# Performance work log

Hardware: AMD Instinct MI355X
Metric: run time of the kernel (lower is better)

## Reference

```python
import jax, jax.numpy as jnp
import numpy as np

MARGIN = 0.2
NEG_INF = -1e30
POS_INF = 1e30


def setup_inputs() -> dict:
    key = jax.random.key(0)
    k1, k2 = jax.random.split(key)
    B, D = 8192, 128
    im = jax.random.normal(k1, (B, D), dtype=jnp.float32)
    ids = jax.random.randint(k2, (B,), 0, 512, dtype=jnp.int64)
    return {"im": im, "ids": ids}


def reference(im, ids):
    # scores[i, j] = <im_i, im_j>, with the diagonal zeroed (as in the original,
    # which sets scores[j][j] = 0 before mining). Note the positive set includes
    # the anchor itself, so min over positives includes the zeroed diagonal.
    B = im.shape[0]
    scores = im @ im.T                      # [B, B]
    scores = scores * (1.0 - jnp.eye(B, dtype=scores.dtype))
    pos_mask = ids[:, None] == ids[None, :]  # same id (includes self)
    neg_mask = ~pos_mask
    max_neg = jnp.max(jnp.where(neg_mask, scores, NEG_INF), axis=1)  # hardest negative per anchor
    min_pos = jnp.min(jnp.where(pos_mask, scores, POS_INF), axis=1)  # hardest positive per anchor
    cost = jnp.sum(jnp.maximum(MARGIN + max_neg - min_pos, 0.0))
    return cost
```

## Files before the change

kernel.cpp:

```cpp
#include <hip/hip_runtime.h>
#include <hip/hip_bf16.h>

#define MARGIN  0.2f
#define NEG_INF -1e30f
#define POS_INF 1e30f

#define B_SZ 8192
#define D_SZ 128
#define CS   16
#define BLK_COLS 512
#define PHASE_COLS 64
#define NPH (BLK_COLS / PHASE_COLS)
#define NBUF 3

typedef __bf16 bf16x8 __attribute__((ext_vector_type(8)));
typedef float  f32x4  __attribute__((ext_vector_type(4)));
typedef float  f32x16 __attribute__((ext_vector_type(16)));

__global__ __launch_bounds__(256) void k_convert(const float* __restrict__ in,
                                                 __bf16* __restrict__ out) {
    int i = (blockIdx.x * 256 + threadIdx.x) * 8;
    float4 v0 = *reinterpret_cast<const float4*>(in + i);
    float4 v1 = *reinterpret_cast<const float4*>(in + i + 4);
    bf16x8 o;
    o[0] = (__bf16)v0.x; o[1] = (__bf16)v0.y; o[2] = (__bf16)v0.z; o[3] = (__bf16)v0.w;
    o[4] = (__bf16)v1.x; o[5] = (__bf16)v1.y; o[6] = (__bf16)v1.z; o[7] = (__bf16)v1.w;
    *reinterpret_cast<bf16x8*>(out + i) = o;
}

__global__ __launch_bounds__(256, 3) void k_mine(const __bf16* __restrict__ imb,
                                                 const int* __restrict__ ids,
                                                 float* __restrict__ wsmax,
                                                 float* __restrict__ wsmin) {
    __shared__ __bf16 bpanel[NBUF][PHASE_COLS * D_SZ];

    const int bid = blockIdx.x;
    const int wg  = (bid & 7) * 128 + (bid >> 3);
    const int rb  = wg & 63;
    const int cs  = wg >> 6;

    const int tid  = threadIdx.x;
    const int w    = tid >> 6;
    const int lane = tid & 63;
    const int half = lane >> 5;
    const int l5   = lane & 31;

    const int rowbase = rb * 128 + w * 32;
    const int col0    = cs * BLK_COLS;

    const int s_tile = w >> 1;
    const int s_kf0  = (w & 1) * 4;

    bf16x8 afrag[8];
    {
        const __bf16* p = imb + (size_t)(rowbase + l5) * D_SZ + half * 8;
        #pragma unroll
        for (int kf = 0; kf < 8; ++kf)
            afrag[kf] = *reinterpret_cast<const bf16x8*>(p + kf * 16);
    }
    int rid[16];
    #pragma unroll
    for (int r = 0; r < 16; ++r)
        rid[r] = ids[rowbase + (r & 3) + 8 * (r >> 2) + 4 * half];

    #pragma unroll
    for (int pp = 0; pp < 2; ++pp) {
        const __bf16* src = imb + (size_t)(col0 + pp * PHASE_COLS + s_tile * 32 + l5) * D_SZ
                            + s_kf0 * 16 + half * 8;
        #pragma unroll
        for (int j = 0; j < 4; ++j)
            __builtin_amdgcn_global_load_lds(
                (const __attribute__((address_space(1))) unsigned int*)(src + j * 16),
                (__attribute__((address_space(3))) unsigned int*)(&bpanel[pp][(s_tile * 8 + s_kf0 + j) * 512]),
                16, 0, 0);
    }
    asm volatile("s_waitcnt vmcnt(4)" ::: "memory");
    __builtin_amdgcn_s_barrier();

    float mxn[16], mnp[16];
    #pragma unroll
    for (int r = 0; r < 16; ++r) { mxn[r] = NEG_INF; mnp[r] = POS_INF; }

    #pragma unroll 1
    for (int p = 0; p < NPH; ++p) {
        if (p + 2 < NPH) {
            const int bs = (p + 2) % NBUF;
            const __bf16* src = imb + (size_t)(col0 + (p + 2) * PHASE_COLS + s_tile * 32 + l5) * D_SZ
                                + s_kf0 * 16 + half * 8;
            #pragma unroll
            for (int j = 0; j < 4; ++j)
                __builtin_amdgcn_global_load_lds(
                    (const __attribute__((address_space(1))) unsigned int*)(src + j * 16),
                    (__attribute__((address_space(3))) unsigned int*)(&bpanel[bs][(s_tile * 8 + s_kf0 + j) * 512]),
                    16, 0, 0);
        }
        const int buf = p % NBUF;
        #pragma unroll
        for (int t = 0; t < 2; ++t) {
            const __bf16* bbase = &bpanel[buf][t * 4096] + (size_t)lane * 8;
            f32x16 acc = {};
            #pragma unroll
            for (int kf = 0; kf < 8; ++kf) {
                bf16x8 bfr = *reinterpret_cast<const bf16x8*>(bbase + kf * 512);
                acc = __builtin_amdgcn_mfma_f32_32x32x16_bf16(afrag[kf], bfr, acc, 0, 0, 0);
            }
            const int cid = ids[col0 + p * PHASE_COLS + t * 32 + l5];
            #pragma unroll
            for (int r = 0; r < 16; ++r) {
                float sv   = acc[r];
                bool  same = (rid[r] == cid);
                mxn[r] = fmaxf(mxn[r], same ? NEG_INF : sv);
                mnp[r] = fminf(mnp[r], same ? sv : POS_INF);
            }
        }
        if (p + 2 < NPH) {
            asm volatile("s_waitcnt vmcnt(4)" ::: "memory");
        } else {
            asm volatile("s_waitcnt vmcnt(0)" ::: "memory");
        }
        __builtin_amdgcn_s_barrier();
    }

    #pragma unroll
    for (int r = 0; r < 16; ++r) {
        float mx = mxn[r];
        float mn = mnp[r];
        #pragma unroll
        for (int m = 1; m < 32; m <<= 1) {
            mx = fmaxf(mx, __shfl_xor(mx, m, 64));
            mn = fminf(mn, __shfl_xor(mn, m, 64));
        }
        if (l5 == 0) {
            int row = rowbase + (r & 3) + 8 * (r >> 2) + 4 * half;
            wsmax[(size_t)row * CS + cs] = mx;
            wsmin[(size_t)row * CS + cs] = mn;
        }
    }
}

__global__ __launch_bounds__(256) void k_final(const float* __restrict__ wsmax,
                                               const float* __restrict__ wsmin,
                                               float* __restrict__ out) {
    int r = blockIdx.x * 256 + threadIdx.x;
    float mx = NEG_INF;
    float mn = 0.0f;
    #pragma unroll
    for (int c = 0; c < CS; c += 4) {
        f32x4 vx = *reinterpret_cast<const f32x4*>(wsmax + (size_t)r * CS + c);
        f32x4 vn = *reinterpret_cast<const f32x4*>(wsmin + (size_t)r * CS + c);
        mx = fmaxf(mx, fmaxf(fmaxf(vx[0], vx[1]), fmaxf(vx[2], vx[3])));
        mn = fminf(mn, fminf(fminf(vn[0], vn[1]), fminf(vn[2], vn[3])));
    }
    float cost = fmaxf(MARGIN + mx - mn, 0.0f);
    #pragma unroll
    for (int m = 1; m < 64; m <<= 1)
        cost += __shfl_xor(cost, m, 64);
    __shared__ float part[4];
    if ((threadIdx.x & 63) == 0) part[threadIdx.x >> 6] = cost;
    __syncthreads();
    if (threadIdx.x == 0)
        atomicAdd(out, part[0] + part[1] + part[2] + part[3]);
}

extern "C" void kernel_launch(void* const* d_in, const int* in_sizes, int n_in,
                              void* d_out, int out_size, void* d_ws, size_t ws_size,
                              hipStream_t stream) {
    const float* im  = (const float*)d_in[0];
    const int*   ids = (const int*)d_in[1];
    float*       out = (float*)d_out;

    __bf16* imb   = (__bf16*)d_ws;
    float*  wsmax = (float*)((char*)d_ws + (size_t)B_SZ * D_SZ * 2);
    float*  wsmin = wsmax + (size_t)B_SZ * CS;

    hipMemsetAsync(d_out, 0, sizeof(float), stream);

    k_convert<<<(B_SZ * D_SZ) / (256 * 8), 256, 0, stream>>>(im, imb);
    k_mine<<<64 * CS, 256, 0, stream>>>(imb, ids, wsmax, wsmin);
    k_final<<<B_SZ / 256, 256, 0, stream>>>(wsmax, wsmin, out);
}
```

Baseline: 98.65 us.

## Reshape warp tiling to 64x32 per wave so B fragments are reused across two A tiles

Each wave now computes two 32-row subtiles against one 32-column tile, reusing each LDS B fragment for two MFMAs instead of loading it once per MFMA. Column ids are staged in shared memory once per block instead of being read from global memory per phase. Register pressure doubles for A fragments and accumulators, so launch bounds drop to 2 blocks per CU. The partial-result workspace widens to 32 partials per row to hold the per-wave column split.

```diff
diff --git a/kernel.cpp b/kernel.cpp
--- a/kernel.cpp
+++ b/kernel.cpp
@@ -8,6 +8,7 @@
 #define B_SZ 8192
 #define D_SZ 128
 #define CS   16
+#define PCS  32
 #define BLK_COLS 512
 #define PHASE_COLS 64
 #define NPH (BLK_COLS / PHASE_COLS)
@@ -28,11 +29,12 @@
     *reinterpret_cast<bf16x8*>(out + i) = o;
 }
 
-__global__ __launch_bounds__(256, 3) void k_mine(const __bf16* __restrict__ imb,
+__global__ __launch_bounds__(256, 2) void k_mine(const __bf16* __restrict__ imb,
                                                  const int* __restrict__ ids,
                                                  float* __restrict__ wsmax,
                                                  float* __restrict__ wsmin) {
     __shared__ __bf16 bpanel[NBUF][PHASE_COLS * D_SZ];
+    __shared__ int    ids_s[BLK_COLS];
 
     const int bid = blockIdx.x;
     const int wg  = (bid & 7) * 128 + (bid >> 3);
@@ -45,23 +47,32 @@
     const int half = lane >> 5;
     const int l5   = lane & 31;
 
-    const int rowbase = rb * 128 + w * 32;
+    const int h = w >> 1;
+    const int c = w & 1;
+
+    const int rowbase = rb * 128 + h * 64;
     const int col0    = cs * BLK_COLS;
 
     const int s_tile = w >> 1;
     const int s_kf0  = (w & 1) * 4;
 
-    bf16x8 afrag[8];
-    {
-        const __bf16* p = imb + (size_t)(rowbase + l5) * D_SZ + half * 8;
+    *reinterpret_cast<int2*>(&ids_s[tid * 2]) =
+        *reinterpret_cast<const int2*>(ids + col0 + tid * 2);
+
+    bf16x8 afrag[2][8];
+    #pragma unroll
+    for (int st = 0; st < 2; ++st) {
+        const __bf16* p = imb + (size_t)(rowbase + st * 32 + l5) * D_SZ + half * 8;
         #pragma unroll
         for (int kf = 0; kf < 8; ++kf)
-            afrag[kf] = *reinterpret_cast<const bf16x8*>(p + kf * 16);
+            afrag[st][kf] = *reinterpret_cast<const bf16x8*>(p + kf * 16);
     }
-    int rid[16];
+    int rid[2][16];
     #pragma unroll
-    for (int r = 0; r < 16; ++r)
-        rid[r] = ids[rowbase + (r & 3) + 8 * (r >> 2) + 4 * half];
+    for (int st = 0; st < 2; ++st)
+        #pragma unroll
+        for (int r = 0; r < 16; ++r)
+            rid[st][r] = ids[rowbase + st * 32 + (r & 3) + 8 * (r >> 2) + 4 * half];
 
     #pragma unroll
     for (int pp = 0; pp < 2; ++pp) {
@@ -74,12 +85,14 @@
                 (__attribute__((address_space(3))) unsigned int*)(&bpanel[pp][(s_tile * 8 + s_kf0 + j) * 512]),
                 16, 0, 0);
     }
-    asm volatile("s_waitcnt vmcnt(4)" ::: "memory");
+    asm volatile("s_waitcnt vmcnt(4) lgkmcnt(0)" ::: "memory");
     __builtin_amdgcn_s_barrier();
 
-    float mxn[16], mnp[16];
+    float mxn[2][16], mnp[2][16];
     #pragma unroll
-    for (int r = 0; r < 16; ++r) { mxn[r] = NEG_INF; mnp[r] = POS_INF; }
+    for (int st = 0; st < 2; ++st)
+        #pragma unroll
+        for (int r = 0; r < 16; ++r) { mxn[st][r] = NEG_INF; mnp[st][r] = POS_INF; }
 
     #pragma unroll 1
     for (int p = 0; p < NPH; ++p) {
@@ -95,23 +108,25 @@
                     16, 0, 0);
         }
         const int buf = p % NBUF;
+        const int cid = ids_s[p * PHASE_COLS + c * 32 + l5];
+
+        const __bf16* bbase = &bpanel[buf][c * 8 * 512] + (size_t)lane * 8;
+        f32x16 acc0 = {}, acc1 = {};
         #pragma unroll
-        for (int t = 0; t < 2; ++t) {
-            const __bf16* bbase = &bpanel[buf][t * 4096] + (size_t)lane * 8;
-            f32x16 acc = {};
-            #pragma unroll
-            for (int kf = 0; kf < 8; ++kf) {
-                bf16x8 bfr = *reinterpret_cast<const bf16x8*>(bbase + kf * 512);
-                acc = __builtin_amdgcn_mfma_f32_32x32x16_bf16(afrag[kf], bfr, acc, 0, 0, 0);
-            }
-            const int cid = ids[col0 + p * PHASE_COLS + t * 32 + l5];
-            #pragma unroll
-            for (int r = 0; r < 16; ++r) {
-                float sv   = acc[r];
-                bool  same = (rid[r] == cid);
-                mxn[r] = fmaxf(mxn[r], same ? NEG_INF : sv);
-                mnp[r] = fminf(mnp[r], same ? sv : POS_INF);
-            }
+        for (int kf = 0; kf < 8; ++kf) {
+            bf16x8 bfr = *reinterpret_cast<const bf16x8*>(bbase + kf * 512);
+            acc0 = __builtin_amdgcn_mfma_f32_32x32x16_bf16(afrag[0][kf], bfr, acc0, 0, 0, 0);
+            acc1 = __builtin_amdgcn_mfma_f32_32x32x16_bf16(afrag[1][kf], bfr, acc1, 0, 0, 0);
+        }
+        #pragma unroll
+        for (int r = 0; r < 16; ++r) {
+            float s0 = acc0[r], s1 = acc1[r];
+            bool  m0 = (rid[0][r] == cid);
+            bool  m1 = (rid[1][r] == cid);
+            mxn[0][r] = fmaxf(mxn[0][r], m0 ? NEG_INF : s0);
+            mnp[0][r] = fminf(mnp[0][r], m0 ? s0 : POS_INF);
+            mxn[1][r] = fmaxf(mxn[1][r], m1 ? NEG_INF : s1);
+            mnp[1][r] = fminf(mnp[1][r], m1 ? s1 : POS_INF);
         }
         if (p + 2 < NPH) {
             asm volatile("s_waitcnt vmcnt(4)" ::: "memory");
@@ -122,20 +137,22 @@
     }
 
     #pragma unroll
-    for (int r = 0; r < 16; ++r) {
-        float mx = mxn[r];
-        float mn = mnp[r];
+    for (int st = 0; st < 2; ++st)
         #pragma unroll
-        for (int m = 1; m < 32; m <<= 1) {
-            mx = fmaxf(mx, __shfl_xor(mx, m, 64));
-            mn = fminf(mn, __shfl_xor(mn, m, 64));
+        for (int r = 0; r < 16; ++r) {
+            float mx = mxn[st][r];
+            float mn = mnp[st][r];
+            #pragma unroll
+            for (int m = 1; m < 32; m <<= 1) {
+                mx = fmaxf(mx, __shfl_xor(mx, m, 64));
+                mn = fminf(mn, __shfl_xor(mn, m, 64));
+            }
+            if (l5 == 0) {
+                int row = rowbase + st * 32 + (r & 3) + 8 * (r >> 2) + 4 * half;
+                wsmax[(size_t)row * PCS + cs * 2 + c] = mx;
+                wsmin[(size_t)row * PCS + cs * 2 + c] = mn;
+            }
         }
-        if (l5 == 0) {
-            int row = rowbase + (r & 3) + 8 * (r >> 2) + 4 * half;
-            wsmax[(size_t)row * CS + cs] = mx;
-            wsmin[(size_t)row * CS + cs] = mn;
-        }
-    }
 }
 
 __global__ __launch_bounds__(256) void k_final(const float* __restrict__ wsmax,
@@ -145,9 +162,9 @@
     float mx = NEG_INF;
     float mn = 0.0f;
     #pragma unroll
-    for (int c = 0; c < CS; c += 4) {
-        f32x4 vx = *reinterpret_cast<const f32x4*>(wsmax + (size_t)r * CS + c);
-        f32x4 vn = *reinterpret_cast<const f32x4*>(wsmin + (size_t)r * CS + c);
+    for (int cc = 0; cc < PCS; cc += 4) {
+        f32x4 vx = *reinterpret_cast<const f32x4*>(wsmax + (size_t)r * PCS + cc);
+        f32x4 vn = *reinterpret_cast<const f32x4*>(wsmin + (size_t)r * PCS + cc);
         mx = fmaxf(mx, fmaxf(fmaxf(vx[0], vx[1]), fmaxf(vx[2], vx[3])));
         mn = fminf(mn, fminf(fminf(vn[0], vn[1]), fminf(vn[2], vn[3])));
     }
@@ -171,7 +188,7 @@
 
     __bf16* imb   = (__bf16*)d_ws;
     float*  wsmax = (float*)((char*)d_ws + (size_t)B_SZ * D_SZ * 2);
-    float*  wsmin = wsmax + (size_t)B_SZ * CS;
+    float*  wsmin = wsmax + (size_t)B_SZ * PCS;
 
     hipMemsetAsync(d_out, 0, sizeof(float), stream);
 
```

Result: slower. 120.9 us (+22.5%).

## Load B fragments directly from global into registers, dropping LDS staging

Applied to the files above, without the earlier changes.

Replaces the shared-memory triple-buffered B panel (global_load_lds plus barriers) with per-wave register double-buffering: each wave loads its own 32-column B fragments straight from global memory one tile ahead. This removes the LDS traffic and block-wide barriers. In exchange, each of the four waves now fetches the same B columns independently, which quadruples global/L2 reads, and register pressure rises with the extra fragment buffer.

```diff
diff --git a/kernel.cpp b/kernel.cpp
--- a/kernel.cpp
+++ b/kernel.cpp
@@ -8,10 +8,6 @@
 #define B_SZ 8192
 #define D_SZ 128
 #define CS   16
-#define BLK_COLS 512
-#define PHASE_COLS 64
-#define NPH (BLK_COLS / PHASE_COLS)
-#define NBUF 3
 
 typedef __bf16 bf16x8 __attribute__((ext_vector_type(8)));
 typedef float  f32x4  __attribute__((ext_vector_type(4)));
@@ -32,8 +28,6 @@
                                                  const int* __restrict__ ids,
                                                  float* __restrict__ wsmax,
                                                  float* __restrict__ wsmin) {
-    __shared__ __bf16 bpanel[NBUF][PHASE_COLS * D_SZ];
-
     const int bid = blockIdx.x;
     const int wg  = (bid & 7) * 128 + (bid >> 3);
     const int rb  = wg & 63;
@@ -46,10 +40,7 @@
     const int l5   = lane & 31;
 
     const int rowbase = rb * 128 + w * 32;
-    const int col0    = cs * BLK_COLS;
-
-    const int s_tile = w >> 1;
-    const int s_kf0  = (w & 1) * 4;
+    const int col0    = cs * 512;
 
     bf16x8 afrag[8];
     {
@@ -63,62 +54,40 @@
     for (int r = 0; r < 16; ++r)
         rid[r] = ids[rowbase + (r & 3) + 8 * (r >> 2) + 4 * half];
 
-    #pragma unroll
-    for (int pp = 0; pp < 2; ++pp) {
-        const __bf16* src = imb + (size_t)(col0 + pp * PHASE_COLS + s_tile * 32 + l5) * D_SZ
-                            + s_kf0 * 16 + half * 8;
-        #pragma unroll
-        for (int j = 0; j < 4; ++j)
-            __builtin_amdgcn_global_load_lds(
-                (const __attribute__((address_space(1))) unsigned int*)(src + j * 16),
-                (__attribute__((address_space(3))) unsigned int*)(&bpanel[pp][(s_tile * 8 + s_kf0 + j) * 512]),
-                16, 0, 0);
-    }
-    asm volatile("s_waitcnt vmcnt(4)" ::: "memory");
-    __builtin_amdgcn_s_barrier();
-
     float mxn[16], mnp[16];
     #pragma unroll
     for (int r = 0; r < 16; ++r) { mxn[r] = NEG_INF; mnp[r] = POS_INF; }
 
-    #pragma unroll 1
-    for (int p = 0; p < NPH; ++p) {
-        if (p + 2 < NPH) {
-            const int bs = (p + 2) % NBUF;
-            const __bf16* src = imb + (size_t)(col0 + (p + 2) * PHASE_COLS + s_tile * 32 + l5) * D_SZ
-                                + s_kf0 * 16 + half * 8;
+    const __bf16* bp = imb + (size_t)(col0 + l5) * D_SZ + half * 8;
+    bf16x8 bbuf[2][8];
+    int    cidb[2];
+    #pragma unroll
+    for (int kf = 0; kf < 8; ++kf)
+        bbuf[0][kf] = *reinterpret_cast<const bf16x8*>(bp + kf * 16);
+    cidb[0] = ids[col0 + l5];
+
+    #pragma unroll 2
+    for (int t = 0; t < 16; ++t) {
+        const int cur = t & 1;
+        if (t + 1 < 16) {
+            const __bf16* q = bp + (size_t)(t + 1) * 32 * D_SZ;
             #pragma unroll
-            for (int j = 0; j < 4; ++j)
-                __builtin_amdgcn_global_load_lds(
-                    (const __attribute__((address_space(1))) unsigned int*)(src + j * 16),
-                    (__attribute__((address_space(3))) unsigned int*)(&bpanel[bs][(s_tile * 8 + s_kf0 + j) * 512]),
-                    16, 0, 0);
+            for (int kf = 0; kf < 8; ++kf)
+                bbuf[cur ^ 1][kf] = *reinterpret_cast<const bf16x8*>(q + kf * 16);
+            cidb[cur ^ 1] = ids[col0 + (t + 1) * 32 + l5];
         }
-        const int buf = p % NBUF;
+        f32x16 acc = {};
         #pragma unroll
-        for (int t = 0; t < 2; ++t) {
-            const __bf16* bbase = &bpanel[buf][t * 4096] + (size_t)lane * 8;
-            f32x16 acc = {};
-            #pragma unroll
-            for (int kf = 0; kf < 8; ++kf) {
-                bf16x8 bfr = *reinterpret_cast<const bf16x8*>(bbase + kf * 512);
-                acc = __builtin_amdgcn_mfma_f32_32x32x16_bf16(afrag[kf], bfr, acc, 0, 0, 0);
-            }
-            const int cid = ids[col0 + p * PHASE_COLS + t * 32 + l5];
-            #pragma unroll
-            for (int r = 0; r < 16; ++r) {
-                float sv   = acc[r];
-                bool  same = (rid[r] == cid);
-                mxn[r] = fmaxf(mxn[r], same ? NEG_INF : sv);
-                mnp[r] = fminf(mnp[r], same ? sv : POS_INF);
-            }
+        for (int kf = 0; kf < 8; ++kf)
+            acc = __builtin_amdgcn_mfma_f32_32x32x16_bf16(afrag[kf], bbuf[cur][kf], acc, 0, 0, 0);
+        const int cid = cidb[cur];
+        #pragma unroll
+        for (int r = 0; r < 16; ++r) {
+            float sv   = acc[r];
+            bool  same = (rid[r] == cid);
+            mxn[r] = fmaxf(mxn[r], same ? NEG_INF : sv);
+            mnp[r] = fminf(mnp[r], same ? sv : POS_INF);
         }
-        if (p + 2 < NPH) {
-            asm volatile("s_waitcnt vmcnt(4)" ::: "memory");
-        } else {
-            asm volatile("s_waitcnt vmcnt(0)" ::: "memory");
-        }
-        __builtin_amdgcn_s_barrier();
     }
 
     #pragma unroll
```

Result: slower. 153.7 us (+55.8%).
